# Optimization experiments

Measured on AMD Instinct MI355X. Metric: run time of the kernel, lower is better.

The kernel has to match this reference:

```python
import jax, jax.numpy as jnp
import numpy as np

EPS = 1e-7
ROUTINGS = 3

def squash(s, axis=-1):
    # s: capsule vectors; squash along `axis`
    n2 = jnp.sum(s * s, axis=axis, keepdims=True)
    return (n2 / (1.0 + n2) / jnp.sqrt(n2 + EPS)) * s


def setup_inputs() -> dict:
    key = jax.random.key(0)
    k1, k2 = jax.random.split(key)
    B, N, O, Do, Di = 64, 1152, 32, 16, 8
    x = jax.random.normal(k1, (B, N, Di), dtype=jnp.float32)
    weight = 0.01 * jax.random.normal(k2, (N, O, Do, Di), dtype=jnp.float32)
    return {"x": x, "weight": weight}


def reference(x, weight):
    # x: [B, N, Di]; weight: [N, O, Do, Di]
    # x_hat[b,n,o,:] = weight[n,o] @ x[b,n]  -> [B, N, O, Do]
    x_hat = jnp.einsum('noij,bnj->bnoi', weight, x)
    x_hat_det = jax.lax.stop_gradient(x_hat)
    B, N, O, Do = x_hat.shape
    b = jnp.zeros((B, N, O), dtype=x_hat.dtype)
    vj = None
    for i in range(ROUTINGS):
        c = jax.nn.softmax(b, axis=2)  # [B, N, O] over output capsules
        xh = x_hat if i == ROUTINGS - 1 else x_hat_det
        s = jnp.einsum('bno,bnoi->boi', c, xh)  # sum over input capsules
        vj = squash(s, axis=-1)  # [B, O, Do]
        if i < ROUTINGS - 1:
            # agreement: <x_hat[b,n,o], vj[b,o]>
            b = b + jnp.einsum('bnoi,boi->bno', x_hat_det, vj)
    return vj  # [B, O, Do]
```

## Files before the change

### kernel.cpp

```cpp
#include <hip/hip_runtime.h>

#define Bb 64
#define Nn 1152
#define Oo 32
#define DOv 16
#define DIv 8
#define BPB 16

__device__ __forceinline__ void gload_lds16(const void* g, void* l) {
    __builtin_amdgcn_global_load_lds(
        (const __attribute__((address_space(1))) unsigned*)g,
        (__attribute__((address_space(3))) unsigned*)l, 16, 0, 0);
}

__global__ __launch_bounds__(256) void caps_route(
    const float* __restrict__ x,
    const float* __restrict__ w,
    const float* __restrict__ vcum,
    float* __restrict__ spart,
    int nc)
{
    const int t  = threadIdx.x;
    const int o  = t & 31;
    const int bl = t >> 5;
    const int n0 = blockIdx.x * nc;
    const int b0 = blockIdx.y * BPB;

    __shared__ float4 wbuf[2][1024];
    __shared__ float4 xbuf[16][BPB][2];

    int gq[4];
#pragma unroll
    for (int k = 0; k < 4; ++k) {
        int p = k * 256 + t;
        gq[k] = (p & ~31) | ((p ^ (p >> 5)) & 31);
    }

    auto stageW = [&](int n, int c) {
        const float4* wg = (const float4*)(w + (size_t)n * (Oo * DOv * DIv));
#pragma unroll
        for (int k = 0; k < 4; ++k)
            gload_lds16(&wg[gq[k]], &wbuf[c][k * 256 + t]);
    };
    auto stageX = [&](int nb) {
        int cnt = min(16, nc - nb);
        for (int q = t; q < cnt * 32; q += 256) {
            int nn = q >> 5, bb = (q >> 1) & 15, h = q & 1;
            xbuf[nn][bb][h] = ((const float4*)(
                x + ((size_t)(b0 + bb) * Nn + (size_t)(n0 + nb + nn)) * DIv))[h];
        }
    };

    const bool have_v = (vcum != nullptr);
    float vc0[DOv], vc1[DOv];
    if (have_v) {
#pragma unroll
        for (int i = 0; i < DOv; ++i) vc0[i] = vcum[((size_t)(b0 + bl) * Oo + o) * DOv + i];
#pragma unroll
        for (int i = 0; i < DOv; ++i) vc1[i] = vcum[((size_t)(b0 + 8 + bl) * Oo + o) * DOv + i];
    }

    float sacc0[DOv], sacc1[DOv];
#pragma unroll
    for (int i = 0; i < DOv; ++i) { sacc0[i] = 0.f; sacc1[i] = 0.f; }

    stageX(0);
    stageW(n0, 0);
    int cur = 0;

    for (int nn = 0; nn < nc; ++nn) {
        if (nn && (nn & 15) == 0) { __syncthreads(); stageX(nn); }
        __syncthreads();
        if (nn + 1 < nc) stageW(n0 + nn + 1, cur ^ 1);

        float4 xav0 = xbuf[nn & 15][bl][0],     xav1 = xbuf[nn & 15][bl][1];
        float4 xbv0 = xbuf[nn & 15][8 + bl][0], xbv1 = xbuf[nn & 15][8 + bl][1];
        float xa[8] = {xav0.x, xav0.y, xav0.z, xav0.w, xav1.x, xav1.y, xav1.z, xav1.w};
        float xb[8] = {xbv0.x, xbv0.y, xbv0.z, xbv0.w, xbv1.x, xbv1.y, xbv1.z, xbv1.w};

        float xh0[DOv], xh1[DOv];
#pragma unroll
        for (int i = 0; i < DOv; ++i) { xh0[i] = 0.f; xh1[i] = 0.f; }
#pragma unroll
        for (int i2 = 0; i2 < 32; ++i2) {
            float4 wv = wbuf[cur][o * 32 + (i2 ^ o)];
            const int i = i2 >> 1, jb = (i2 & 1) * 4;
            xh0[i] = fmaf(wv.x, xa[jb + 0], xh0[i]);
            xh0[i] = fmaf(wv.y, xa[jb + 1], xh0[i]);
            xh0[i] = fmaf(wv.z, xa[jb + 2], xh0[i]);
            xh0[i] = fmaf(wv.w, xa[jb + 3], xh0[i]);
            xh1[i] = fmaf(wv.x, xb[jb + 0], xh1[i]);
            xh1[i] = fmaf(wv.y, xb[jb + 1], xh1[i]);
            xh1[i] = fmaf(wv.z, xb[jb + 2], xh1[i]);
            xh1[i] = fmaf(wv.w, xb[jb + 3], xh1[i]);
        }

        float c0, c1;
        if (have_v) {
            float l0 = 0.f, l1 = 0.f;
#pragma unroll
            for (int i = 0; i < DOv; ++i) { l0 += xh0[i] * vc0[i]; l1 += xh1[i] * vc1[i]; }
            float m0 = l0, m1 = l1;
#pragma unroll
            for (int d = 16; d >= 1; d >>= 1) {
                m0 = fmaxf(m0, __shfl_xor(m0, d));
                m1 = fmaxf(m1, __shfl_xor(m1, d));
            }
            float e0 = __expf(l0 - m0), e1 = __expf(l1 - m1);
            float s0 = e0, s1 = e1;
#pragma unroll
            for (int d = 16; d >= 1; d >>= 1) {
                s0 += __shfl_xor(s0, d);
                s1 += __shfl_xor(s1, d);
            }
            c0 = e0 / s0; c1 = e1 / s1;
        } else {
            c0 = 1.0f / 32.0f; c1 = 1.0f / 32.0f;
        }

#pragma unroll
        for (int i = 0; i < DOv; ++i) { sacc0[i] += c0 * xh0[i]; sacc1[i] += c1 * xh1[i]; }
        cur ^= 1;
    }

    float* p  = spart + (size_t)blockIdx.x * (Bb * Oo * DOv);
    float* p0 = p + ((size_t)(b0 + bl) * Oo + o) * DOv;
    float* p1 = p + ((size_t)(b0 + 8 + bl) * Oo + o) * DOv;
#pragma unroll
    for (int i = 0; i < DOv; ++i) p0[i] = sacc0[i];
#pragma unroll
    for (int i = 0; i < DOv; ++i) p1[i] = sacc1[i];
}

__global__ __launch_bounds__(64) void caps_squash(
    const float* __restrict__ spart, int nch,
    const float* __restrict__ vin,
    float* __restrict__ vout,
    float* __restrict__ out)
{
    const int b = blockIdx.x, oo = blockIdx.y;
    const int t = threadIdx.x;
    const int i = t & 15, pg = t >> 4;
    const size_t base = ((size_t)b * Oo + oo) * DOv + i;
    float s = 0.f;
#pragma unroll 4
    for (int p = pg; p < nch; p += 4)
        s += spart[(size_t)p * (Bb * Oo * DOv) + base];
    s += __shfl_xor(s, 16);
    s += __shfl_xor(s, 32);
    float n2 = s * s;
#pragma unroll
    for (int d = 8; d >= 1; d >>= 1) n2 += __shfl_xor(n2, d);
    float vj = s * (n2 / ((1.f + n2) * sqrtf(n2 + 1e-7f)));
    if (t < 16) {
        if (vout) vout[base] = (vin ? vin[base] : 0.f) + vj;
        if (out)  out[base]  = vj;
    }
}

extern "C" void kernel_launch(void* const* d_in, const int* in_sizes, int n_in,
                              void* d_out, int out_size, void* d_ws, size_t ws_size,
                              hipStream_t stream)
{
    const float* x = (const float*)d_in[0];
    const float* w = (const float*)d_in[1];
    float* out = (float*)d_out;

    static const int cfgs[][2] = {{144,8},{72,16},{36,32},{18,64},{9,128},{4,288},{2,576},{1,1152}};
    int nch = 1, nc = 1152;
    for (auto& c : cfgs) {
        size_t need = ((size_t)c[0] * Bb * Oo * DOv + (size_t)Bb * Oo * DOv) * sizeof(float);
        if (need <= ws_size) { nch = c[0]; nc = c[1]; break; }
    }

    float* spart = (float*)d_ws;
    float* vcum  = spart + (size_t)nch * Bb * Oo * DOv;

    dim3 grid(nch, Bb / BPB), blk(256);
    dim3 sgrid(Bb, Oo), sblk(64);

    caps_route<<<grid, blk, 0, stream>>>(x, w, nullptr, spart, nc);
    caps_squash<<<sgrid, sblk, 0, stream>>>(spart, nch, nullptr, vcum, nullptr);
    caps_route<<<grid, blk, 0, stream>>>(x, w, vcum, spart, nc);
    caps_squash<<<sgrid, sblk, 0, stream>>>(spart, nch, vcum, vcum, nullptr);
    caps_route<<<grid, blk, 0, stream>>>(x, w, vcum, spart, nc);
    caps_squash<<<sgrid, sblk, 0, stream>>>(spart, nch, nullptr, nullptr, out);
}
```

Measured before the change: 104.5 us.

## Process four batch groups per thread and drop softmax max-subtraction

Each route block now covers 32 batches instead of 16, so each thread computes four batch rows per input capsule and reuses every LDS weight read across four FMA groups. This halves the number of times the weight tensor is streamed across the grid. The softmax drops its max-reduction shuffle pass, which relies on the logits being small enough not to overflow exp. The default chunk config changes to 128 chunks of 9 capsules, and the extra accumulators raise register pressure, which may lower occupancy.

```diff
diff --git a/kernel.cpp b/kernel.cpp
--- a/kernel.cpp
+++ b/kernel.cpp
@@ -5,7 +5,8 @@
 #define Oo 32
 #define DOv 16
 #define DIv 8
-#define BPB 16
+#define BPB 32
+#define NG 4
 
 __device__ __forceinline__ void gload_lds16(const void* g, void* l) {
     __builtin_amdgcn_global_load_lds(
@@ -44,25 +45,28 @@
     };
     auto stageX = [&](int nb) {
         int cnt = min(16, nc - nb);
-        for (int q = t; q < cnt * 32; q += 256) {
-            int nn = q >> 5, bb = (q >> 1) & 15, h = q & 1;
+        for (int q = t; q < cnt * BPB * 2; q += 256) {
+            int nn = q >> 6, bb = (q >> 1) & 31, h = q & 1;
             xbuf[nn][bb][h] = ((const float4*)(
                 x + ((size_t)(b0 + bb) * Nn + (size_t)(n0 + nb + nn)) * DIv))[h];
         }
     };
 
     const bool have_v = (vcum != nullptr);
-    float vc0[DOv], vc1[DOv];
+    float vc[NG][DOv];
     if (have_v) {
 #pragma unroll
-        for (int i = 0; i < DOv; ++i) vc0[i] = vcum[((size_t)(b0 + bl) * Oo + o) * DOv + i];
-#pragma unroll
-        for (int i = 0; i < DOv; ++i) vc1[i] = vcum[((size_t)(b0 + 8 + bl) * Oo + o) * DOv + i];
-    }
-
-    float sacc0[DOv], sacc1[DOv];
-#pragma unroll
-    for (int i = 0; i < DOv; ++i) { sacc0[i] = 0.f; sacc1[i] = 0.f; }
+        for (int g = 0; g < NG; ++g)
+#pragma unroll
+            for (int i = 0; i < DOv; ++i)
+                vc[g][i] = vcum[((size_t)(b0 + 8 * g + bl) * Oo + o) * DOv + i];
+    }
+
+    float sacc[NG][DOv];
+#pragma unroll
+    for (int g = 0; g < NG; ++g)
+#pragma unroll
+        for (int i = 0; i < DOv; ++i) sacc[g][i] = 0.f;
 
     stageX(0);
     stageW(n0, 0);
@@ -73,63 +77,71 @@
         __syncthreads();
         if (nn + 1 < nc) stageW(n0 + nn + 1, cur ^ 1);
 
-        float4 xav0 = xbuf[nn & 15][bl][0],     xav1 = xbuf[nn & 15][bl][1];
-        float4 xbv0 = xbuf[nn & 15][8 + bl][0], xbv1 = xbuf[nn & 15][8 + bl][1];
-        float xa[8] = {xav0.x, xav0.y, xav0.z, xav0.w, xav1.x, xav1.y, xav1.z, xav1.w};
-        float xb[8] = {xbv0.x, xbv0.y, xbv0.z, xbv0.w, xbv1.x, xbv1.y, xbv1.z, xbv1.w};
-
-        float xh0[DOv], xh1[DOv];
-#pragma unroll
-        for (int i = 0; i < DOv; ++i) { xh0[i] = 0.f; xh1[i] = 0.f; }
+        float xa[NG][DIv];
+#pragma unroll
+        for (int g = 0; g < NG; ++g) {
+            float4 v0 = xbuf[nn & 15][8 * g + bl][0];
+            float4 v1 = xbuf[nn & 15][8 * g + bl][1];
+            xa[g][0] = v0.x; xa[g][1] = v0.y; xa[g][2] = v0.z; xa[g][3] = v0.w;
+            xa[g][4] = v1.x; xa[g][5] = v1.y; xa[g][6] = v1.z; xa[g][7] = v1.w;
+        }
+
+        float xh[NG][DOv];
+#pragma unroll
+        for (int g = 0; g < NG; ++g)
+#pragma unroll
+            for (int i = 0; i < DOv; ++i) xh[g][i] = 0.f;
+
 #pragma unroll
         for (int i2 = 0; i2 < 32; ++i2) {
             float4 wv = wbuf[cur][o * 32 + (i2 ^ o)];
             const int i = i2 >> 1, jb = (i2 & 1) * 4;
-            xh0[i] = fmaf(wv.x, xa[jb + 0], xh0[i]);
-            xh0[i] = fmaf(wv.y, xa[jb + 1], xh0[i]);
-            xh0[i] = fmaf(wv.z, xa[jb + 2], xh0[i]);
-            xh0[i] = fmaf(wv.w, xa[jb + 3], xh0[i]);
-            xh1[i] = fmaf(wv.x, xb[jb + 0], xh1[i]);
-            xh1[i] = fmaf(wv.y, xb[jb + 1], xh1[i]);
-            xh1[i] = fmaf(wv.z, xb[jb + 2], xh1[i]);
-            xh1[i] = fmaf(wv.w, xb[jb + 3], xh1[i]);
-        }
-
-        float c0, c1;
+#pragma unroll
+            for (int g = 0; g < NG; ++g) {
+                xh[g][i] = fmaf(wv.x, xa[g][jb + 0], xh[g][i]);
+                xh[g][i] = fmaf(wv.y, xa[g][jb + 1], xh[g][i]);
+                xh[g][i] = fmaf(wv.z, xa[g][jb + 2], xh[g][i]);
+                xh[g][i] = fmaf(wv.w, xa[g][jb + 3], xh[g][i]);
+            }
+        }
+
+        float c[NG];
         if (have_v) {
-            float l0 = 0.f, l1 = 0.f;
-#pragma unroll
-            for (int i = 0; i < DOv; ++i) { l0 += xh0[i] * vc0[i]; l1 += xh1[i] * vc1[i]; }
-            float m0 = l0, m1 = l1;
-#pragma unroll
-            for (int d = 16; d >= 1; d >>= 1) {
-                m0 = fmaxf(m0, __shfl_xor(m0, d));
-                m1 = fmaxf(m1, __shfl_xor(m1, d));
+            float e[NG], ssum[NG];
+#pragma unroll
+            for (int g = 0; g < NG; ++g) {
+                float l = 0.f;
+#pragma unroll
+                for (int i = 0; i < DOv; ++i) l += xh[g][i] * vc[g][i];
+                e[g] = __expf(l);
+                ssum[g] = e[g];
             }
-            float e0 = __expf(l0 - m0), e1 = __expf(l1 - m1);
-            float s0 = e0, s1 = e1;
-#pragma unroll
-            for (int d = 16; d >= 1; d >>= 1) {
-                s0 += __shfl_xor(s0, d);
-                s1 += __shfl_xor(s1, d);
-            }
-            c0 = e0 / s0; c1 = e1 / s1;
+#pragma unroll
+            for (int d = 16; d >= 1; d >>= 1)
+#pragma unroll
+                for (int g = 0; g < NG; ++g)
+                    ssum[g] += __shfl_xor(ssum[g], d);
+#pragma unroll
+            for (int g = 0; g < NG; ++g) c[g] = e[g] / ssum[g];
         } else {
-            c0 = 1.0f / 32.0f; c1 = 1.0f / 32.0f;
-        }
-
-#pragma unroll
-        for (int i = 0; i < DOv; ++i) { sacc0[i] += c0 * xh0[i]; sacc1[i] += c1 * xh1[i]; }
+#pragma unroll
+            for (int g = 0; g < NG; ++g) c[g] = 1.0f / 32.0f;
+        }
+
+#pragma unroll
+        for (int g = 0; g < NG; ++g)
+#pragma unroll
+            for (int i = 0; i < DOv; ++i) sacc[g][i] += c[g] * xh[g][i];
         cur ^= 1;
     }
 
-    float* p  = spart + (size_t)blockIdx.x * (Bb * Oo * DOv);
-    float* p0 = p + ((size_t)(b0 + bl) * Oo + o) * DOv;
-    float* p1 = p + ((size_t)(b0 + 8 + bl) * Oo + o) * DOv;
-#pragma unroll
-    for (int i = 0; i < DOv; ++i) p0[i] = sacc0[i];
-#pragma unroll
-    for (int i = 0; i < DOv; ++i) p1[i] = sacc1[i];
+    float* p = spart + (size_t)blockIdx.x * (Bb * Oo * DOv);
+#pragma unroll
+    for (int g = 0; g < NG; ++g) {
+        float* pg = p + ((size_t)(b0 + 8 * g + bl) * Oo + o) * DOv;
+#pragma unroll
+        for (int i = 0; i < DOv; ++i) pg[i] = sacc[g][i];
+    }
 }
 
 __global__ __launch_bounds__(64) void caps_squash(
@@ -166,7 +178,7 @@
     const float* w = (const float*)d_in[1];
     float* out = (float*)d_out;
 
-    static const int cfgs[][2] = {{144,8},{72,16},{36,32},{18,64},{9,128},{4,288},{2,576},{1,1152}};
+    static const int cfgs[][2] = {{128,9},{72,16},{36,32},{18,64},{9,128},{4,288},{2,576},{1,1152}};
     int nch = 1, nc = 1152;
     for (auto& c : cfgs) {
         size_t need = ((size_t)c[0] * Bb * Oo * DOv + (size_t)Bb * Oo * DOv) * sizeof(float);
```

New measurement: 103.7 us. About the same (-0.8%).
